# Performance work log

Hardware: AMD Instinct MI355X
Metric: run time of the kernel (lower is better)

Reference implementation:

```python
import jax, jax.numpy as jnp
import numpy as np

N = 4096      # num_nodes
D_IN = 768    # input_dim
HID = 512     # hidden_dim per head
D_OUT = 768   # output_dim
H = 4         # num_heads
ALPHA = 0.2   # LeakyReLU slope
NEG_BIG = -9e15


def _layer_norm(x, g, b, eps=1e-5):
    m = jnp.mean(x, axis=-1, keepdims=True)
    v = jnp.var(x, axis=-1, keepdims=True)
    return (x - m) * jax.lax.rsqrt(v + eps) * g + b


def _multihead_gat(h, mask, ew, W, a, concat):
    # h: [N, F_in], W: [H, F_in, O], a: [H, 2*O], mask/ew: [N, N]
    O = W.shape[-1]
    Wh = jnp.einsum('nf,hfo->hno', h, W)                      # [H, N, O]
    # e[h,i,j] = leakyrelu(a1.Wh[i] + a2.Wh[j]) -- equivalent to the
    # concat(Wh_i, Wh_j) @ a formulation, without the O(N^2 * 2O) tensor.
    s_src = jnp.einsum('hno,ho->hn', Wh, a[:, :O])            # [H, N]
    s_dst = jnp.einsum('hno,ho->hn', Wh, a[:, O:])            # [H, N]
    e = jax.nn.leaky_relu(s_src[:, :, None] + s_dst[:, None, :], negative_slope=ALPHA)
    att = jnp.where(mask[None], e, NEG_BIG)
    if ew is not None:
        att = att * ew[None]                                   # faithful: scale AFTER masking
    att = jax.nn.softmax(att, axis=-1)                         # dropout is identity at eval
    hp = jnp.einsum('hnm,hmo->hno', att, Wh)                   # [H, N, O]
    if concat:
        return jax.nn.elu(jnp.transpose(hp, (1, 0, 2)).reshape(h.shape[0], H * O))
    return jnp.mean(hp, axis=0)                                # concat=False: mean, no ELU


def setup_inputs() -> dict:
    key = jax.random.key(0)
    ks = jax.random.split(key, 10)
    return {
        'node_features': jax.random.normal(ks[0], (N, D_IN), jnp.float32),
        'adjacency': jax.random.randint(ks[1], (N, N), 0, 2, jnp.int32),
        'edge_weights': jax.random.uniform(ks[2], (N, N), jnp.float32),
        'W0': (jax.random.normal(ks[3], (H, D_IN, HID)) * 0.05).astype(jnp.float32),
        'a0': (jax.random.normal(ks[4], (H, 2 * HID)) * 0.05).astype(jnp.float32),
        'W1': (jax.random.normal(ks[5], (H, HID * H, D_OUT)) * 0.02).astype(jnp.float32),
        'a1': (jax.random.normal(ks[6], (H, 2 * D_OUT)) * 0.05).astype(jnp.float32),
        'rp0_w': (jax.random.normal(ks[7], (D_IN, HID * H)) * 0.02).astype(jnp.float32),
        'rp0_b': jnp.zeros((HID * H,), jnp.float32),
        'rp1_w': (jax.random.normal(ks[8], (HID * H, D_OUT)) * 0.02).astype(jnp.float32),
        'rp1_b': jnp.zeros((D_OUT,), jnp.float32),
        'ln0_g': jnp.ones((HID * H,), jnp.float32),
        'ln0_b': jnp.zeros((HID * H,), jnp.float32),
        'ln1_g': jnp.ones((D_OUT,), jnp.float32),
        'ln1_b': jnp.zeros((D_OUT,), jnp.float32),
    }


def reference(node_features, adjacency, edge_weights, W0, a0, W1, a1,
              rp0_w, rp0_b, rp1_w, rp1_b, ln0_g, ln0_b, ln1_g, ln1_b):
    n = node_features.shape[0]
    adj = adjacency.astype(jnp.float32) + jnp.eye(n, dtype=jnp.float32)  # add self-loops
    mask = adj > 0
    h = node_features
    # layer 0: concat heads -> [N, H*HID], residual projection, LN, ELU (dropout=identity)
    h1 = _multihead_gat(h, mask, edge_weights, W0, a0, concat=True)
    h1 = h1 + (h @ rp0_w + rp0_b)
    h1 = _layer_norm(h1, ln0_g, ln0_b)
    h1 = jax.nn.elu(h1)
    # layer 1 (last): mean over heads -> [N, D_OUT], residual projection, LN
    h2 = _multihead_gat(h1, mask, edge_weights, W1, a1, concat=False)
    h2 = h2 + (h1 @ rp1_w + rp1_b)
    h2 = _layer_norm(h2, ln1_g, ln1_b)
    return h2
```

## Files before the change

kernel.cpp:

```cpp
#include <hip/hip_runtime.h>


typedef unsigned short u16;
typedef unsigned char u8;
typedef unsigned long long u64;
using short8  = __attribute__((ext_vector_type(8))) short;
using float4v = __attribute__((ext_vector_type(4))) float;
using int4v   = __attribute__((ext_vector_type(4))) int;
using int8v   = __attribute__((ext_vector_type(8))) int;

#define NN 4096
#define NHEADS 4

__device__ __forceinline__ u16 f2bf(float f) {
  union { float f; unsigned u; } v; v.f = f;
  unsigned u = v.u;
  return (u16)((u + 0x7FFFu + ((u >> 16) & 1u)) >> 16);
}
__device__ __forceinline__ float bf2f(u16 x) {
  union { unsigned u; float f; } v; v.u = ((unsigned)x) << 16; return v.f;
}
__device__ __forceinline__ unsigned pk_fp8x4(float a, float b, float c, float d) {
  int lo = __builtin_amdgcn_cvt_pk_fp8_f32(a, b, 0, false);
  return (unsigned)__builtin_amdgcn_cvt_pk_fp8_f32(c, d, lo, true);
}

__device__ __forceinline__ void async16(const void* g, void* l) {
  __builtin_amdgcn_global_load_lds(
      (const __attribute__((address_space(1))) unsigned int*)g,
      (__attribute__((address_space(3))) unsigned int*)l, 16, 0, 0);
}

__global__ __launch_bounds__(256) void cast_f32_bf16(const float* __restrict__ in,
                                                     u16* __restrict__ out, int n) {
  int i = blockIdx.x * 256 + threadIdx.x;
  if (i < n) out[i] = f2bf(in[i]);
}

__global__ __launch_bounds__(256) void adj2bits(const int* __restrict__ adj,
                                                u64* __restrict__ bits) {
  size_t gw = (size_t)blockIdx.x * 4 + (threadIdx.x >> 6);
  int lane = threadIdx.x & 63;
  int v = adj[gw * 64 + lane];
  u64 b = __ballot(v != 0);
  if (lane == 0) bits[gw] = b;
}

__global__ __launch_bounds__(256) void transcast_f32(const float* __restrict__ in,
                                                     u16* __restrict__ out, int R, int C) {
  __shared__ float t[32][33];
  size_t zoff = (size_t)blockIdx.z * R * C;
  in += zoff; out += zoff;
  int c0 = blockIdx.x * 32, r0 = blockIdx.y * 32;
  int tx = threadIdx.x & 31, ty = threadIdx.x >> 5;
#pragma unroll
  for (int i = 0; i < 32; i += 8)
    t[ty + i][tx] = in[(size_t)(r0 + ty + i) * C + (c0 + tx)];
  __syncthreads();
#pragma unroll
  for (int i = 0; i < 32; i += 8)
    out[(size_t)(c0 + ty + i) * R + (r0 + tx)] = f2bf(t[tx][ty + i]);
}

__global__ __launch_bounds__(256) void wa_kernel(const float* __restrict__ W,
                                                 const float* __restrict__ a,
                                                 float* __restrict__ wa, int F, int O) {
  int gw = blockIdx.x * 4 + (threadIdx.x >> 6);
  int lane = threadIdx.x & 63;
  int total = 2 * NHEADS * F;
  if (gw >= total) return;
  int side = gw / (NHEADS * F);
  int rem = gw - side * NHEADS * F;
  int h = rem / F, f = rem - h * F;
  const float* wrow = W + ((size_t)h * F + f) * O;
  const float* av = a + (size_t)h * 2 * O + (size_t)side * O;
  float s = 0.f;
  for (int o = lane; o < O; o += 64) s += wrow[o] * av[o];
#pragma unroll
  for (int off = 32; off > 0; off >>= 1) s += __shfl_down(s, off);
  if (lane == 0) wa[gw] = s;
}

__global__ __launch_bounds__(256) void s8_kernel_f32(const float* __restrict__ X,
                                                     const float* __restrict__ wa,
                                                     float* __restrict__ sout, int F) {
  int n = blockIdx.x * 4 + (threadIdx.x >> 6);
  int lane = threadIdx.x & 63;
  const float* x = X + (size_t)n * F;
  float acc[8] = {};
  for (int f = lane; f < F; f += 64) {
    float xv = x[f];
#pragma unroll
    for (int k = 0; k < 8; k++) acc[k] += xv * wa[(size_t)k * F + f];
  }
#pragma unroll
  for (int k = 0; k < 8; k++) {
    float s = acc[k];
#pragma unroll
    for (int off = 32; off > 0; off >>= 1) s += __shfl_down(s, off);
    if (lane == 0) sout[(size_t)k * NN + n] = s;
  }
}

__global__ __launch_bounds__(256) void s8_kernel_bf16(const u16* __restrict__ X,
                                                      const float* __restrict__ wa,
                                                      float* __restrict__ sout, int F) {
  int n = blockIdx.x * 4 + (threadIdx.x >> 6);
  int lane = threadIdx.x & 63;
  const u16* x = X + (size_t)n * F;
  float acc[8] = {};
  for (int f = lane; f < F; f += 64) {
    float xv = bf2f(x[f]);
#pragma unroll
    for (int k = 0; k < 8; k++) acc[k] += xv * wa[(size_t)k * F + f];
  }
#pragma unroll
  for (int k = 0; k < 8; k++) {
    float s = acc[k];
#pragma unroll
    for (int off = 32; off > 0; off >>= 1) s += __shfl_down(s, off);
    if (lane == 0) sout[(size_t)k * NN + n] = s;
  }
}

__global__ __launch_bounds__(256) void sdmax_kernel(const float* __restrict__ s,
                                                    float* __restrict__ out) {
  int h = blockIdx.x, tid = threadIdx.x;
  const float* sd = s + (size_t)(NHEADS + h) * NN;
  float m = -3e38f;
  for (int i = tid; i < NN; i += 256) m = fmaxf(m, sd[i]);
  __shared__ float red[4];
#pragma unroll
  for (int off = 32; off > 0; off >>= 1) m = fmaxf(m, __shfl_down(m, off));
  if ((tid & 63) == 0) red[tid >> 6] = m;
  __syncthreads();
  if (tid == 0) out[h] = fmaxf(fmaxf(red[0], red[1]), fmaxf(red[2], red[3]));
}

template <int G>
__global__ __launch_bounds__(256) void pexp_g_kernel(const u64* __restrict__ mb,
                                                     const float* __restrict__ ew,
                                                     const float* __restrict__ s,
                                                     const float* __restrict__ sdmax,
                                                     u8* __restrict__ P,
                                                     float* __restrict__ L, int hb) {
  __shared__ u64 mrow[64];
  __shared__ float lred[G][4];
  int i = blockIdx.x, tid = threadIdx.x;
  if (tid < 64) mrow[tid] = mb[(size_t)i * 64 + tid];
  float sr[G], mp[G], lacc[G];
#pragma unroll
  for (int z = 0; z < G; z++) {
    sr[z] = s[(size_t)(hb + z) * NN + i];
    mp[z] = fmaxf(0.0f, sr[z] + sdmax[hb + z]);
    lacc[z] = 0.f;
  }
  const float4* wrow = (const float4*)(ew + (size_t)i * NN);
  __syncthreads();
  for (int jv = tid; jv < NN / 4; jv += 256) {
    float4 w = wrow[jv];
    int j0 = jv * 4;
    u64 mw = mrow[jv >> 4] >> (j0 & 63);
    float we[4]; we[0] = w.x; we[1] = w.y; we[2] = w.z; we[3] = w.w;
    bool m[4];
#pragma unroll
    for (int k = 0; k < 4; k++) m[k] = ((mw >> k) & 1ull) || (j0 + k == i);
#pragma unroll
    for (int z = 0; z < G; z++) {
      const float4 sd4 = *(const float4*)(s + (size_t)(NHEADS + hb + z) * NN + j0);
      float sd[4]; sd[0] = sd4.x; sd[1] = sd4.y; sd[2] = sd4.z; sd[3] = sd4.w;
      float p[4];
#pragma unroll
      for (int k = 0; k < 4; k++) {
        float x = sr[z] + sd[k];
        float e = x > 0.f ? x : 0.2f * x;
        float v = (m[k] ? e : -9e15f) * we[k];
        p[k] = __expf(v - mp[z]);
        lacc[z] += p[k];
      }
      *(unsigned*)(P + ((size_t)z * NN + i) * NN + j0) = pk_fp8x4(p[0], p[1], p[2], p[3]);
    }
  }
#pragma unroll
  for (int z = 0; z < G; z++) {
    float r = lacc[z];
#pragma unroll
    for (int off = 32; off > 0; off >>= 1) r += __shfl_down(r, off);
    if ((tid & 63) == 0) lred[z][tid >> 6] = r;
  }
  __syncthreads();
  if (tid < G)
    L[(size_t)(hb + tid) * NN + i] = lred[tid][0] + lred[tid][1] + lred[tid][2] + lred[tid][3];
}

#define LDA_(CUR, MH)                                                            \
  _Pragma("unroll") for (int mi = 0; mi < 4; mi++) {                             \
    int lr = mi * 32 + wm16 + lm;                                                \
    int sw = lr & 7;                                                             \
    const u16* ap = &LA[CUR][MH][lr * 64];                                       \
    aR[mi][0] = *(const short8*)(ap + ((quad ^ sw) * 8));                        \
    aR[mi][1] = *(const short8*)(ap + (((4 + quad) ^ sw) * 8));                  \
  }

#define LDB_(CUR, NH)                                                            \
  _Pragma("unroll") for (int ni = 0; ni < 2; ni++) {                             \
    int lc = ni * 64 + wn16 + lm;                                                \
    int sw = lc & 7;                                                             \
    const u16* bp = &LB[CUR][NH][lc * 64];                                       \
    bR[NH][ni][0] = *(const short8*)(bp + ((quad ^ sw) * 8));                    \
    bR[NH][ni][1] = *(const short8*)(bp + (((4 + quad) ^ sw) * 8));              \
  }

#define VMW4 asm volatile("s_waitcnt vmcnt(4)" ::: "memory")
#define VMW0 asm volatile("s_waitcnt vmcnt(0)" ::: "memory")

#define PH(MH, NH, LOADA, LOADB, STAGE, WAIT)                                    \
  {                                                                              \
    LOADA;                                                                       \
    LOADB;                                                                       \
    STAGE;                                                                       \
    WAIT;                                                                        \
    __builtin_amdgcn_s_barrier();                                                \
    __builtin_amdgcn_s_setprio(1);                                               \
    _Pragma("unroll") for (int mi = 0; mi < 4; mi++)                             \
      _Pragma("unroll") for (int ni = 0; ni < 2; ni++) {                         \
        acc[MH * 4 + mi][NH * 2 + ni] = __builtin_amdgcn_mfma_f32_16x16x32_bf16( \
            aR[mi][0], bR[NH][ni][0], acc[MH * 4 + mi][NH * 2 + ni], 0, 0, 0);   \
        acc[MH * 4 + mi][NH * 2 + ni] = __builtin_amdgcn_mfma_f32_16x16x32_bf16( \
            aR[mi][1], bR[NH][ni][1], acc[MH * 4 + mi][NH * 2 + ni], 0, 0, 0);   \
      }                                                                          \
    __builtin_amdgcn_s_setprio(0);                                               \
    __builtin_amdgcn_s_barrier();                                                \
  }

__global__ __launch_bounds__(512, 2) void gemm_proj(const u16* __restrict__ A,
                                                    const u16* __restrict__ Bt,
                                                    u8* __restrict__ F8T,
                                                    float* __restrict__ F32,
                                                    const float* __restrict__ bias,
                                                    int K, int split, int ldcF) {
  int lin = blockIdx.y * 16 + blockIdx.x;
  int nwg = gridDim.y * 16;
  int cpx = nwg >> 3;
  int swz = (lin & 7) * cpx + (lin >> 3);
  int row0 = (swz & 15) * 256;
  int col0 = (swz >> 4) * 256;

  __shared__ u16 LA[2][2][8192];
  __shared__ u16 LB[2][2][8192];

  int tid = threadIdx.x;
  int wave = tid >> 6, lane = tid & 63;
  int wm = wave >> 2, wn = wave & 3;
  int wm16 = wm * 16, wn16 = wn * 16;
  int lm = lane & 15, quad = lane >> 4;

  int r0 = tid >> 3;
  int cg = (tid & 7) ^ (r0 & 7);
  const u16* aSrc = A + (size_t)(row0 + r0) * K + cg * 8;
  const u16* bSrc = Bt + (size_t)(col0 + r0) * K + cg * 8;

  auto stA = [&](int d, int h, int kt) {
    const u16* p = aSrc + (size_t)h * 128 * K + (size_t)kt * 64;
    async16(p, &LA[d][h][wave * 512]);
    async16(p + (size_t)64 * K, &LA[d][h][4096 + wave * 512]);
  };
  auto stB = [&](int d, int h, int kt) {
    const u16* p = bSrc + (size_t)h * 128 * K + (size_t)kt * 64;
    async16(p, &LB[d][h][wave * 512]);
    async16(p + (size_t)64 * K, &LB[d][h][4096 + wave * 512]);
  };

  float4v acc[8][4] = {};
  short8 aR[4][2];
  short8 bR[2][2][2];

  const int NT = K >> 6;
  const int NI = NT >> 1;

  stB(0, 0, 0); stA(0, 0, 0); stA(0, 1, 0); stB(0, 1, 0);
  stB(1, 0, 1); stA(1, 0, 1);
  VMW4;
  __builtin_amdgcn_s_barrier();

  for (int i = 0; i < NI - 1; i++) {
    int kt1 = 2 * i + 1, kt2 = 2 * i + 2, kt3 = 2 * i + 3;
    PH(0, 0, LDA_(0, 0), LDB_(0, 0), stA(1, 1, kt1), ((void)0));
    PH(0, 1, ((void)0),  LDB_(0, 1), stB(1, 1, kt1), ((void)0));
    PH(1, 1, LDA_(0, 1), ((void)0),  stB(0, 0, kt2), ((void)0));
    PH(1, 0, ((void)0),  ((void)0),  stA(0, 0, kt2), VMW4);
    PH(0, 0, LDA_(1, 0), LDB_(1, 0), stA(0, 1, kt2), ((void)0));
    PH(0, 1, ((void)0),  LDB_(1, 1), stB(0, 1, kt2), ((void)0));
    PH(1, 1, LDA_(1, 1), ((void)0),  stB(1, 0, kt3), ((void)0));
    PH(1, 0, ((void)0),  ((void)0),  stA(1, 0, kt3), VMW4);
  }
  {
    int kt1 = NT - 1;
    PH(0, 0, LDA_(0, 0), LDB_(0, 0), stA(1, 1, kt1), ((void)0));
    PH(0, 1, ((void)0),  LDB_(0, 1), stB(1, 1, kt1), ((void)0));
    PH(1, 1, LDA_(0, 1), ((void)0),  ((void)0),      ((void)0));
    PH(1, 0, ((void)0),  ((void)0),  ((void)0),      VMW0);
    PH(0, 0, LDA_(1, 0), LDB_(1, 0), ((void)0),      ((void)0));
    PH(0, 1, ((void)0),  LDB_(1, 1), ((void)0),      ((void)0));
    PH(1, 1, LDA_(1, 1), ((void)0),  ((void)0),      ((void)0));
    PH(1, 0, ((void)0),  ((void)0),  ((void)0),      ((void)0));
  }

  if (col0 < split) {
#pragma unroll
    for (int m = 0; m < 8; m++) {
#pragma unroll
      for (int n = 0; n < 4; n++) {
        int grow0 = row0 + m * 32 + wm16 + quad * 4;
        int gcol = col0 + n * 64 + wn16 + lm;
        unsigned pk = pk_fp8x4(acc[m][n][0], acc[m][n][1], acc[m][n][2], acc[m][n][3]);
        *(unsigned*)&F8T[(size_t)gcol * NN + grow0] = pk;
      }
    }
  } else {
#pragma unroll
    for (int m = 0; m < 8; m++) {
#pragma unroll
      for (int n = 0; n < 4; n++) {
#pragma unroll
        for (int r = 0; r < 4; r++) {
          int grow = row0 + m * 32 + wm16 + quad * 4 + r;
          int gcol = col0 + n * 64 + wn16 + lm - split;
          F32[(size_t)grow * ldcF + gcol] = acc[m][n][r] + bias[gcol];
        }
      }
    }
  }
}
#undef PH
#undef VMW4
#undef VMW0
#undef LDA_
#undef LDB_

template <int MODE>
__global__ __launch_bounds__(256) void gemm_mx(const u8* __restrict__ A,
                                               const u8* __restrict__ Bt,
                                               float* __restrict__ Cout,
                                               int ldc, int coloff_base, int coloff_step,
                                               size_t bStride, size_t cStride) {
  constexpr int K = NN;
  int h = blockIdx.z;
  const u8* Ab = A + (size_t)h * ((size_t)NN * NN);
  const u8* Bb = Bt + (size_t)h * bStride;
  int row0 = blockIdx.x * 128;
  int col0 = blockIdx.y * 128;
  int coloff = coloff_base + h * coloff_step;

  __shared__ u8 ldsA[2][128 * 128];
  __shared__ u8 ldsB[2][128 * 128];

  int tid = threadIdx.x;
  int wave = tid >> 6, lane = tid & 63;
  int wm = wave >> 1, wn = wave & 1;
  int lm = lane & 15, quad = lane >> 4;

  int sr = tid >> 3, sc = tid & 7;
  int scg = sc ^ (sr & 7);
  const u8* aPtr = Ab + (size_t)(row0 + sr) * K + scg * 16;
  const u8* bPtr = Bb + (size_t)(col0 + sr) * K + scg * 16;
  const size_t rowStep = (size_t)32 * K;

  float4v acc[4][4] = {};

  auto stage = [&](int buf, int k0) {
    u8* la = &ldsA[buf][wave * 1024];
    u8* lb = &ldsB[buf][wave * 1024];
#pragma unroll
    for (int b = 0; b < 4; b++) {
      async16(aPtr + k0 + b * rowStep, la + b * 4096);
      async16(bPtr + k0 + b * rowStep, lb + b * 4096);
    }
  };

  const int nt = K >> 7;
  stage(0, 0);
  stage(1, 128);
  asm volatile("s_waitcnt vmcnt(8)" ::: "memory");
  __builtin_amdgcn_s_barrier();
  __builtin_amdgcn_sched_barrier(0);

  for (int t = 0; t < nt; t++) {
    int cur = t & 1;
    const u8* LA = ldsA[cur];
    const u8* LB = ldsB[cur];
    int8v a32[4], b32[4];
#pragma unroll
    for (int s = 0; s < 4; s++) {
      int ra = wm * 64 + s * 16 + lm;
      int rb = wn * 64 + s * 16 + lm;
      int swa = ra & 7, swb = rb & 7;
      int4v alo = *(const int4v*)(&LA[ra * 128 + (((2 * quad) ^ swa) * 16)]);
      int4v ahi = *(const int4v*)(&LA[ra * 128 + (((2 * quad + 1) ^ swa) * 16)]);
      int4v blo = *(const int4v*)(&LB[rb * 128 + (((2 * quad) ^ swb) * 16)]);
      int4v bhi = *(const int4v*)(&LB[rb * 128 + (((2 * quad + 1) ^ swb) * 16)]);
      a32[s][0] = alo[0]; a32[s][1] = alo[1]; a32[s][2] = alo[2]; a32[s][3] = alo[3];
      a32[s][4] = ahi[0]; a32[s][5] = ahi[1]; a32[s][6] = ahi[2]; a32[s][7] = ahi[3];
      b32[s][0] = blo[0]; b32[s][1] = blo[1]; b32[s][2] = blo[2]; b32[s][3] = blo[3];
      b32[s][4] = bhi[0]; b32[s][5] = bhi[1]; b32[s][6] = bhi[2]; b32[s][7] = bhi[3];
    }
#pragma unroll
    for (int i = 0; i < 4; i++)
#pragma unroll
      for (int j = 0; j < 4; j++)
        acc[i][j] = __builtin_amdgcn_mfma_scale_f32_16x16x128_f8f6f4(
            a32[i], b32[j], acc[i][j], 0, 0, 0, 127, 0, 127);
    __builtin_amdgcn_s_barrier();
    __builtin_amdgcn_sched_barrier(0);
    if (t + 2 < nt) {
      stage(cur, (t + 2) << 7);
      asm volatile("s_waitcnt vmcnt(8)" ::: "memory");
    } else {
      asm volatile("s_waitcnt vmcnt(0)" ::: "memory");
    }
    __builtin_amdgcn_s_barrier();
    __builtin_amdgcn_sched_barrier(0);
  }

#pragma unroll
  for (int i = 0; i < 4; i++) {
#pragma unroll
    for (int j = 0; j < 4; j++) {
#pragma unroll
      for (int r = 0; r < 4; r++) {
        int grow = row0 + wm * 64 + i * 16 + quad * 4 + r;
        int gcol = col0 + wn * 64 + j * 16 + lm;
        float v = acc[i][j][r];
        if constexpr (MODE == 2) {
          Cout[(size_t)grow * ldc + coloff + gcol] = v;
        } else {
          Cout[(size_t)h * cStride + (size_t)grow * ldc + gcol] = v;
        }
      }
    }
  }
}

__global__ __launch_bounds__(256) void ln0_kernel(const float* __restrict__ accin,
                                                  const float* __restrict__ rp,
                                                  const float* __restrict__ Lsum,
                                                  const float* __restrict__ g,
                                                  const float* __restrict__ b,
                                                  u16* __restrict__ h1b) {
  const int C = 2048;
  int n = blockIdx.x, tid = threadIdx.x;
  __shared__ float xs[2048];
  __shared__ float red[2][4];
  __shared__ float mrs[2];
  float linv[NHEADS];
#pragma unroll
  for (int h = 0; h < NHEADS; h++) linv[h] = 1.0f / Lsum[(size_t)h * NN + n];
  float sum = 0.f, sq = 0.f;
  const float* ar = accin + (size_t)n * C;
  const float* rr = rp + (size_t)n * C;
  for (int c = tid; c < C; c += 256) {
    float v = ar[c] * linv[c >> 9];
    v = v > 0.f ? v : (__expf(v) - 1.f);
    float x = v + rr[c];
    xs[c] = x; sum += x; sq += x * x;
  }
#pragma unroll
  for (int off = 32; off > 0; off >>= 1) { sum += __shfl_down(sum, off); sq += __shfl_down(sq, off); }
  if ((tid & 63) == 0) { red[0][tid >> 6] = sum; red[1][tid >> 6] = sq; }
  __syncthreads();
  if (tid == 0) {
    float s = red[0][0] + red[0][1] + red[0][2] + red[0][3];
    float q = red[1][0] + red[1][1] + red[1][2] + red[1][3];
    float mean = s / C, var = q / C - mean * mean;
    mrs[0] = mean; mrs[1] = rsqrtf(var + 1e-5f);
  }
  __syncthreads();
  float mean = mrs[0], rstd = mrs[1];
  for (int c = tid; c < C; c += 256) {
    float y = (xs[c] - mean) * rstd * g[c] + b[c];
    float z = y > 0.f ? y : (__expf(y) - 1.f);
    h1b[(size_t)n * C + c] = f2bf(z);
  }
}

__global__ __launch_bounds__(256) void ln1_kernel(const float* __restrict__ hp1,
                                                  const float* __restrict__ rp1,
                                                  const float* __restrict__ Lsum,
                                                  const float* __restrict__ g,
                                                  const float* __restrict__ b,
                                                  float* __restrict__ out) {
  const int C = 768;
  int n = blockIdx.x, tid = threadIdx.x;
  __shared__ float xs[768];
  __shared__ float red[2][4];
  __shared__ float mrs[2];
  float linv[NHEADS];
#pragma unroll
  for (int h = 0; h < NHEADS; h++) linv[h] = 0.25f / Lsum[(size_t)h * NN + n];
  float sum = 0.f, sq = 0.f;
  for (int c = tid; c < C; c += 256) {
    float x = hp1[((size_t)0 * NN + n) * C + c] * linv[0] +
              hp1[((size_t)1 * NN + n) * C + c] * linv[1] +
              hp1[((size_t)2 * NN + n) * C + c] * linv[2] +
              hp1[((size_t)3 * NN + n) * C + c] * linv[3];
    x += rp1[(size_t)n * C + c];
    xs[c] = x; sum += x; sq += x * x;
  }
#pragma unroll
  for (int off = 32; off > 0; off >>= 1) { sum += __shfl_down(sum, off); sq += __shfl_down(sq, off); }
  if ((tid & 63) == 0) { red[0][tid >> 6] = sum; red[1][tid >> 6] = sq; }
  __syncthreads();
  if (tid == 0) {
    float s = red[0][0] + red[0][1] + red[0][2] + red[0][3];
    float q = red[1][0] + red[1][1] + red[1][2] + red[1][3];
    float mean = s / C, var = q / C - mean * mean;
    mrs[0] = mean; mrs[1] = rsqrtf(var + 1e-5f);
  }
  __syncthreads();
  float mean = mrs[0], rstd = mrs[1];
  for (int c = tid; c < C; c += 256)
    out[(size_t)n * C + c] = (xs[c] - mean) * rstd * g[c] + b[c];
}

extern "C" void kernel_launch(void* const* d_in, const int* in_sizes, int n_in,
                              void* d_out, int out_size, void* d_ws, size_t ws_size,
                              hipStream_t stream) {
  (void)in_sizes; (void)n_in; (void)out_size;
  const float* X    = (const float*)d_in[0];
  const int*   adj  = (const int*)d_in[1];
  const float* ew   = (const float*)d_in[2];
  const float* W0   = (const float*)d_in[3];
  const float* a0   = (const float*)d_in[4];
  const float* W1   = (const float*)d_in[5];
  const float* a1   = (const float*)d_in[6];
  const float* rp0w = (const float*)d_in[7];
  const float* rp0b = (const float*)d_in[8];
  const float* rp1w = (const float*)d_in[9];
  const float* rp1b = (const float*)d_in[10];
  const float* ln0g = (const float*)d_in[11];
  const float* ln0b = (const float*)d_in[12];
  const float* ln1g = (const float*)d_in[13];
  const float* ln1b = (const float*)d_in[14];
  float* out = (float*)d_out;
  char* wsb = (char*)d_ws;

  constexpr size_t OFF_XBF   = 0;
  constexpr size_t OFF_W0T   = 6291456;
  constexpr size_t OFF_RP0WT = 9437184;
  constexpr size_t OFF_W1T   = 12582912;
  constexpr size_t OFF_RP1WT = 25165824;
  constexpr size_t OFF_WA0   = 28311552;
  constexpr size_t OFF_WA1   = 28336128;
  constexpr size_t OFF_S0    = 28401664;
  constexpr size_t OFF_S1    = 28532736;
  constexpr size_t OFF_L0    = 28664320;
  constexpr size_t OFF_L1    = 28729856;
  constexpr size_t OFF_H1B   = 28795392;
  constexpr size_t D         = 45572608;
  constexpr size_t PD        = D + 50331648;
  constexpr size_t PN        = (size_t)NN * NN;
  constexpr size_t OFF_HP1   = PD + 4 * PN;
  constexpr size_t OFF_MASK  = 213344768;
  constexpr size_t OFF_SM0   = 215441920;
  constexpr size_t OFF_SM1   = 215442176;

  u16*   XBF   = (u16*)(wsb + OFF_XBF);
  u16*   W0T   = (u16*)(wsb + OFF_W0T);
  u16*   RP0WT = (u16*)(wsb + OFF_RP0WT);
  u16*   W1T   = (u16*)(wsb + OFF_W1T);
  u16*   RP1WT = (u16*)(wsb + OFF_RP1WT);
  float* WA0   = (float*)(wsb + OFF_WA0);
  float* WA1   = (float*)(wsb + OFF_WA1);
  float* S0    = (float*)(wsb + OFF_S0);
  float* S1    = (float*)(wsb + OFF_S1);
  float* L0    = (float*)(wsb + OFF_L0);
  float* L1    = (float*)(wsb + OFF_L1);
  u16*   H1B   = (u16*)(wsb + OFF_H1B);
  u8*    WH0T  = (u8*)(wsb + D);
  float* RP0   = (float*)(wsb + D + 16777216);
  u8*    WH1T  = (u8*)(wsb + D);
  float* RP1   = (float*)(wsb + D + 25165824);
  u8*    P     = (u8*)(wsb + PD);
  float* HP1   = (float*)(wsb + OFF_HP1);
  float* ACC0  = (float*)(wsb + OFF_HP1);
  u64*   MASK  = (u64*)(wsb + OFF_MASK);
  float* SM0   = (float*)(wsb + OFF_SM0);
  float* SM1   = (float*)(wsb + OFF_SM1);

  const int G = (ws_size >= OFF_HP1 + 50331648) ? 4 : 1;

  adj2bits<<<dim3(65536), 256, 0, stream>>>(adj, MASK);
  cast_f32_bf16<<<dim3((NN * 768 + 255) / 256), 256, 0, stream>>>(X, XBF, NN * 768);
  transcast_f32<<<dim3(16, 24, 4), 256, 0, stream>>>(W0, W0T, 768, 512);
  transcast_f32<<<dim3(24, 64, 4), 256, 0, stream>>>(W1, W1T, 2048, 768);
  transcast_f32<<<dim3(64, 24, 1), 256, 0, stream>>>(rp0w, RP0WT, 768, 2048);
  transcast_f32<<<dim3(24, 64, 1), 256, 0, stream>>>(rp1w, RP1WT, 2048, 768);

  wa_kernel<<<dim3(2 * NHEADS * 768 / 4), 256, 0, stream>>>(W0, a0, WA0, 768, 512);
  s8_kernel_f32<<<dim3(NN / 4), 256, 0, stream>>>(X, WA0, S0, 768);
  sdmax_kernel<<<dim3(NHEADS), 256, 0, stream>>>(S0, SM0);

  gemm_proj<<<dim3(16, 16), 512, 0, stream>>>(XBF, W0T, WH0T, RP0, rp0b, 768, 2048, 2048);

  for (int g = 0; g < NHEADS; g += G) {
    if (G == 4) pexp_g_kernel<4><<<dim3(NN), 256, 0, stream>>>(MASK, ew, S0, SM0, P, L0, g);
    else        pexp_g_kernel<1><<<dim3(NN), 256, 0, stream>>>(MASK, ew, S0, SM0, P, L0, g);
    gemm_mx<2><<<dim3(32, 4, G), 256, 0, stream>>>(P, WH0T + (size_t)g * 512 * NN,
        ACC0, 2048, g * 512, 512, (size_t)512 * NN, 0);
  }
  ln0_kernel<<<dim3(NN), 256, 0, stream>>>(ACC0, RP0, L0, ln0g, ln0b, H1B);

  wa_kernel<<<dim3(2 * NHEADS * 2048 / 4), 256, 0, stream>>>(W1, a1, WA1, 2048, 768);
  s8_kernel_bf16<<<dim3(NN / 4), 256, 0, stream>>>(H1B, WA1, S1, 2048);
  sdmax_kernel<<<dim3(NHEADS), 256, 0, stream>>>(S1, SM1);

  gemm_proj<<<dim3(16, 15), 512, 0, stream>>>(H1B, W1T, WH1T, RP1, rp1b, 2048, 3072, 768);

  for (int g = 0; g < NHEADS; g += G) {
    if (G == 4) pexp_g_kernel<4><<<dim3(NN), 256, 0, stream>>>(MASK, ew, S1, SM1, P, L1, g);
    else        pexp_g_kernel<1><<<dim3(NN), 256, 0, stream>>>(MASK, ew, S1, SM1, P, L1, g);
    gemm_mx<3><<<dim3(32, 6, G), 256, 0, stream>>>(P, WH1T + (size_t)g * 768 * NN,
        HP1 + (size_t)g * NN * 768, 768, 0, 0, (size_t)768 * NN, (size_t)NN * 768);
  }
  ln1_kernel<<<dim3(NN), 256, 0, stream>>>(HP1, RP1, L1, ln1g, ln1b, out);
}
```

Measured before the change: 579.0 us.

## Restructure FP8 attention GEMM into 256x128 tiles with phased async pipeline

The MX fp8 P@Wh GEMM moves from 128x128 tiles with 4 waves to 256x128 tiles with 8 waves (512 threads, two blocks per CU). The K loop is split into 8 sub-phases per two K tiles, and each phase interleaves LDS fragment loads, async global-to-LDS staging of half-tiles, and four MFMAs under s_setprio. This mirrors the existing gemm_proj schedule. The aim is more operand reuse per block and better overlap of memory traffic with MFMA work, at the cost of more barriers, larger LDS use and a more fragile wait-count schedule.

```diff
diff --git a/kernel.cpp b/kernel.cpp
--- a/kernel.cpp
+++ b/kernel.cpp
@@ -338,99 +338,128 @@
 #undef LDA_
 #undef LDB_
 
+#define MXLDA_(CUR, MH)                                                          \
+  _Pragma("unroll") for (int mi = 0; mi < 4; mi++) {                             \
+    int lr = mi * 32 + wm16 + lm;                                                \
+    int sw = lr & 7;                                                             \
+    const u8* ap = &LA[CUR][MH][lr * 128];                                       \
+    int4v lo = *(const int4v*)(ap + (((2 * quad) ^ sw) * 16));                   \
+    int4v hi = *(const int4v*)(ap + (((2 * quad + 1) ^ sw) * 16));               \
+    aR[mi][0] = lo[0]; aR[mi][1] = lo[1]; aR[mi][2] = lo[2]; aR[mi][3] = lo[3];  \
+    aR[mi][4] = hi[0]; aR[mi][5] = hi[1]; aR[mi][6] = hi[2]; aR[mi][7] = hi[3];  \
+  }
+
+#define MXLDB_(CUR, NH)                                                          \
+  {                                                                              \
+    int lc = wn16 + lm;                                                          \
+    int sw = lc & 7;                                                             \
+    const u8* bp = &LB[CUR][NH][lc * 128];                                       \
+    int4v lo = *(const int4v*)(bp + (((2 * quad) ^ sw) * 16));                   \
+    int4v hi = *(const int4v*)(bp + (((2 * quad + 1) ^ sw) * 16));               \
+    bR[NH][0] = lo[0]; bR[NH][1] = lo[1]; bR[NH][2] = lo[2]; bR[NH][3] = lo[3];  \
+    bR[NH][4] = hi[0]; bR[NH][5] = hi[1]; bR[NH][6] = hi[2]; bR[NH][7] = hi[3];  \
+  }
+
+#define MXVMW3 asm volatile("s_waitcnt vmcnt(3)" ::: "memory")
+#define MXVMW0 asm volatile("s_waitcnt vmcnt(0)" ::: "memory")
+
+#define MXPH(MH, NH, LOADA, LOADB, STAGE, WAIT)                                  \
+  {                                                                              \
+    LOADA;                                                                       \
+    LOADB;                                                                       \
+    STAGE;                                                                       \
+    WAIT;                                                                        \
+    __builtin_amdgcn_s_barrier();                                                \
+    __builtin_amdgcn_s_setprio(1);                                               \
+    _Pragma("unroll") for (int mi = 0; mi < 4; mi++)                             \
+      acc[MH * 4 + mi][NH] = __builtin_amdgcn_mfma_scale_f32_16x16x128_f8f6f4(   \
+          aR[mi], bR[NH], acc[MH * 4 + mi][NH], 0, 0, 0, 127, 0, 127);           \
+    __builtin_amdgcn_s_setprio(0);                                               \
+    __builtin_amdgcn_s_barrier();                                                \
+  }
+
 template <int MODE>
-__global__ __launch_bounds__(256) void gemm_mx(const u8* __restrict__ A,
-                                               const u8* __restrict__ Bt,
-                                               float* __restrict__ Cout,
-                                               int ldc, int coloff_base, int coloff_step,
-                                               size_t bStride, size_t cStride) {
+__global__ __launch_bounds__(512, 2) void gemm_mx(const u8* __restrict__ A,
+                                                  const u8* __restrict__ Bt,
+                                                  float* __restrict__ Cout,
+                                                  int ldc, int coloff_base, int coloff_step,
+                                                  size_t bStride, size_t cStride) {
   constexpr int K = NN;
   int h = blockIdx.z;
   const u8* Ab = A + (size_t)h * ((size_t)NN * NN);
   const u8* Bb = Bt + (size_t)h * bStride;
-  int row0 = blockIdx.x * 128;
+  int row0 = blockIdx.x * 256;
   int col0 = blockIdx.y * 128;
   int coloff = coloff_base + h * coloff_step;
 
-  __shared__ u8 ldsA[2][128 * 128];
-  __shared__ u8 ldsB[2][128 * 128];
+  __shared__ u8 LA[2][2][16384];
+  __shared__ u8 LB[2][2][8192];
 
   int tid = threadIdx.x;
   int wave = tid >> 6, lane = tid & 63;
-  int wm = wave >> 1, wn = wave & 1;
+  int wm = wave >> 2, wn = wave & 3;
+  int wm16 = wm * 16, wn16 = wn * 16;
   int lm = lane & 15, quad = lane >> 4;
 
-  int sr = tid >> 3, sc = tid & 7;
-  int scg = sc ^ (sr & 7);
-  const u8* aPtr = Ab + (size_t)(row0 + sr) * K + scg * 16;
-  const u8* bPtr = Bb + (size_t)(col0 + sr) * K + scg * 16;
-  const size_t rowStep = (size_t)32 * K;
-
-  float4v acc[4][4] = {};
-
-  auto stage = [&](int buf, int k0) {
-    u8* la = &ldsA[buf][wave * 1024];
-    u8* lb = &ldsB[buf][wave * 1024];
-#pragma unroll
-    for (int b = 0; b < 4; b++) {
-      async16(aPtr + k0 + b * rowStep, la + b * 4096);
-      async16(bPtr + k0 + b * rowStep, lb + b * 4096);
-    }
+  int r0 = tid >> 3;
+  int cg = (tid & 7) ^ (r0 & 7);
+  const u8* aSrc = Ab + (size_t)(row0 + r0) * K + cg * 16;
+  const u8* bSrc = Bb + (size_t)(col0 + r0) * K + cg * 16;
+
+  auto stA = [&](int d, int hh, int kt) {
+    const u8* p = aSrc + (size_t)hh * 128 * K + (size_t)kt * 128;
+    async16(p, &LA[d][hh][wave * 1024]);
+    async16(p + (size_t)64 * K, &LA[d][hh][8192 + wave * 1024]);
   };
-
-  const int nt = K >> 7;
-  stage(0, 0);
-  stage(1, 128);
-  asm volatile("s_waitcnt vmcnt(8)" ::: "memory");
+  auto stB = [&](int d, int hh, int kt) {
+    const u8* p = bSrc + (size_t)hh * 64 * K + (size_t)kt * 128;
+    async16(p, &LB[d][hh][wave * 1024]);
+  };
+
+  float4v acc[8][2] = {};
+  int8v aR[4];
+  int8v bR[2];
+
+  const int NT = K >> 7;
+  const int NI = NT >> 1;
+
+  stB(0, 0, 0); stA(0, 0, 0); stA(0, 1, 0); stB(0, 1, 0);
+  stB(1, 0, 1); stA(1, 0, 1);
+  MXVMW3;
   __builtin_amdgcn_s_barrier();
-  __builtin_amdgcn_sched_barrier(0);
-
-  for (int t = 0; t < nt; t++) {
-    int cur = t & 1;
-    const u8* LA = ldsA[cur];
-    const u8* LB = ldsB[cur];
-    int8v a32[4], b32[4];
-#pragma unroll
-    for (int s = 0; s < 4; s++) {
-      int ra = wm * 64 + s * 16 + lm;
-      int rb = wn * 64 + s * 16 + lm;
-      int swa = ra & 7, swb = rb & 7;
-      int4v alo = *(const int4v*)(&LA[ra * 128 + (((2 * quad) ^ swa) * 16)]);
-      int4v ahi = *(const int4v*)(&LA[ra * 128 + (((2 * quad + 1) ^ swa) * 16)]);
-      int4v blo = *(const int4v*)(&LB[rb * 128 + (((2 * quad) ^ swb) * 16)]);
-      int4v bhi = *(const int4v*)(&LB[rb * 128 + (((2 * quad + 1) ^ swb) * 16)]);
-      a32[s][0] = alo[0]; a32[s][1] = alo[1]; a32[s][2] = alo[2]; a32[s][3] = alo[3];
-      a32[s][4] = ahi[0]; a32[s][5] = ahi[1]; a32[s][6] = ahi[2]; a32[s][7] = ahi[3];
-      b32[s][0] = blo[0]; b32[s][1] = blo[1]; b32[s][2] = blo[2]; b32[s][3] = blo[3];
-      b32[s][4] = bhi[0]; b32[s][5] = bhi[1]; b32[s][6] = bhi[2]; b32[s][7] = bhi[3];
-    }
-#pragma unroll
-    for (int i = 0; i < 4; i++)
-#pragma unroll
-      for (int j = 0; j < 4; j++)
-        acc[i][j] = __builtin_amdgcn_mfma_scale_f32_16x16x128_f8f6f4(
-            a32[i], b32[j], acc[i][j], 0, 0, 0, 127, 0, 127);
-    __builtin_amdgcn_s_barrier();
-    __builtin_amdgcn_sched_barrier(0);
-    if (t + 2 < nt) {
-      stage(cur, (t + 2) << 7);
-      asm volatile("s_waitcnt vmcnt(8)" ::: "memory");
-    } else {
-      asm volatile("s_waitcnt vmcnt(0)" ::: "memory");
-    }
-    __builtin_amdgcn_s_barrier();
-    __builtin_amdgcn_sched_barrier(0);
-  }
-
-#pragma unroll
-  for (int i = 0; i < 4; i++) {
-#pragma unroll
-    for (int j = 0; j < 4; j++) {
+
+  for (int i = 0; i < NI - 1; i++) {
+    int kt1 = 2 * i + 1, kt2 = 2 * i + 2, kt3 = 2 * i + 3;
+    MXPH(0, 0, MXLDA_(0, 0), MXLDB_(0, 0), stA(1, 1, kt1), ((void)0));
+    MXPH(0, 1, ((void)0),    MXLDB_(0, 1), stB(1, 1, kt1), ((void)0));
+    MXPH(1, 1, MXLDA_(0, 1), ((void)0),    stB(0, 0, kt2), ((void)0));
+    MXPH(1, 0, ((void)0),    ((void)0),    stA(0, 0, kt2), MXVMW3);
+    MXPH(0, 0, MXLDA_(1, 0), MXLDB_(1, 0), stA(0, 1, kt2), ((void)0));
+    MXPH(0, 1, ((void)0),    MXLDB_(1, 1), stB(0, 1, kt2), ((void)0));
+    MXPH(1, 1, MXLDA_(1, 1), ((void)0),    stB(1, 0, kt3), ((void)0));
+    MXPH(1, 0, ((void)0),    ((void)0),    stA(1, 0, kt3), MXVMW3);
+  }
+  {
+    int kt1 = NT - 1;
+    MXPH(0, 0, MXLDA_(0, 0), MXLDB_(0, 0), stA(1, 1, kt1), ((void)0));
+    MXPH(0, 1, ((void)0),    MXLDB_(0, 1), stB(1, 1, kt1), ((void)0));
+    MXPH(1, 1, MXLDA_(0, 1), ((void)0),    ((void)0),      ((void)0));
+    MXPH(1, 0, ((void)0),    ((void)0),    ((void)0),      MXVMW0);
+    MXPH(0, 0, MXLDA_(1, 0), MXLDB_(1, 0), ((void)0),      ((void)0));
+    MXPH(0, 1, ((void)0),    MXLDB_(1, 1), ((void)0),      ((void)0));
+    MXPH(1, 1, MXLDA_(1, 1), ((void)0),    ((void)0),      ((void)0));
+    MXPH(1, 0, ((void)0),    ((void)0),    ((void)0),      ((void)0));
+  }
+
+#pragma unroll
+  for (int m = 0; m < 8; m++) {
+#pragma unroll
+    for (int n = 0; n < 2; n++) {
 #pragma unroll
       for (int r = 0; r < 4; r++) {
-        int grow = row0 + wm * 64 + i * 16 + quad * 4 + r;
-        int gcol = col0 + wn * 64 + j * 16 + lm;
-        float v = acc[i][j][r];
+        int grow = row0 + m * 32 + wm16 + quad * 4 + r;
+        int gcol = col0 + n * 64 + wn16 + lm;
+        float v = acc[m][n][r];
         if constexpr (MODE == 2) {
           Cout[(size_t)grow * ldc + coloff + gcol] = v;
         } else {
@@ -440,6 +469,11 @@
     }
   }
 }
+#undef MXPH
+#undef MXVMW3
+#undef MXVMW0
+#undef MXLDA_
+#undef MXLDB_
 
 __global__ __launch_bounds__(256) void ln0_kernel(const float* __restrict__ accin,
                                                   const float* __restrict__ rp,
@@ -605,7 +639,7 @@
   for (int g = 0; g < NHEADS; g += G) {
     if (G == 4) pexp_g_kernel<4><<<dim3(NN), 256, 0, stream>>>(MASK, ew, S0, SM0, P, L0, g);
     else        pexp_g_kernel<1><<<dim3(NN), 256, 0, stream>>>(MASK, ew, S0, SM0, P, L0, g);
-    gemm_mx<2><<<dim3(32, 4, G), 256, 0, stream>>>(P, WH0T + (size_t)g * 512 * NN,
+    gemm_mx<2><<<dim3(16, 4, G), 512, 0, stream>>>(P, WH0T + (size_t)g * 512 * NN,
         ACC0, 2048, g * 512, 512, (size_t)512 * NN, 0);
   }
   ln0_kernel<<<dim3(NN), 256, 0, stream>>>(ACC0, RP0, L0, ln0g, ln0b, H1B);
@@ -619,7 +653,7 @@
   for (int g = 0; g < NHEADS; g += G) {
     if (G == 4) pexp_g_kernel<4><<<dim3(NN), 256, 0, stream>>>(MASK, ew, S1, SM1, P, L1, g);
     else        pexp_g_kernel<1><<<dim3(NN), 256, 0, stream>>>(MASK, ew, S1, SM1, P, L1, g);
-    gemm_mx<3><<<dim3(32, 6, G), 256, 0, stream>>>(P, WH1T + (size_t)g * 768 * NN,
+    gemm_mx<3><<<dim3(16, 6, G), 512, 0, stream>>>(P, WH1T + (size_t)g * 768 * NN,
         HP1 + (size_t)g * NN * 768, 768, 0, 0, (size_t)768 * NN, (size_t)NN * 768);
   }
   ln1_kernel<<<dim3(NN), 256, 0, stream>>>(HP1, RP1, L1, ln1g, ln1b, out);
```

Result: slower. 631.1 us (+9.0%).
